# Optimization experiments

Measured on AMD Instinct MI355X. Metric: run time of the kernel, lower is better.

## Reference

```python
import jax, jax.numpy as jnp
import numpy as np
import math

NUM_GROUPS = 8
NUM_HEADS = 4
EPS = 1e-5


def group_norm(x, gamma, beta):
    B, C, H, W = x.shape
    g = x.reshape(B, NUM_GROUPS, C // NUM_GROUPS, H, W)
    mean = g.mean(axis=(2, 3, 4), keepdims=True)
    var = g.var(axis=(2, 3, 4), keepdims=True)
    g = (g - mean) * jax.lax.rsqrt(var + EPS)
    x = g.reshape(B, C, H, W)
    return x * gamma[None, :, None, None] + beta[None, :, None, None]


def setup_inputs() -> dict:
    key = jax.random.key(0)
    ks = jax.random.split(key, 4)
    B, C, H, W = 4, 256, 64, 64
    x = jax.random.normal(ks[0], (B, C, H, W), dtype=jnp.float32)
    gamma = jnp.ones((C,), dtype=jnp.float32)
    beta = jnp.zeros((C,), dtype=jnp.float32)
    w_qkv = jax.random.normal(ks[1], (3 * C, C), dtype=jnp.float32) / math.sqrt(C)
    b_qkv = jnp.zeros((3 * C,), dtype=jnp.float32)
    w_proj = jax.random.normal(ks[2], (C, C), dtype=jnp.float32) / math.sqrt(C)
    b_proj = jnp.zeros((C,), dtype=jnp.float32)
    return {"x": x, "gamma": gamma, "beta": beta, "w_qkv": w_qkv,
            "b_qkv": b_qkv, "w_proj": w_proj, "b_proj": b_proj}


def reference(x, gamma, beta, w_qkv, b_qkv, w_proj, b_proj):
    B, C, H, W = x.shape
    hd = C // NUM_HEADS  # head dim
    h = group_norm(x, gamma, beta)
    # 1x1 conv == per-pixel matmul: [B,3C,H,W]
    qkv = jnp.einsum('bchw,oc->bohw', h, w_qkv) + b_qkv[None, :, None, None]
    q, k, v = jnp.split(qkv, 3, axis=1)

    def shape(t):
        # [B,C,H,W] -> [B, heads, HW, hd]
        return t.reshape(B, NUM_HEADS, hd, H * W).transpose(0, 1, 3, 2)

    q, k, v = shape(q), shape(k), shape(v)
    attn = jnp.einsum('bhqd,bhkd->bhqk', q, k) * (1.0 / math.sqrt(hd))
    attn = jax.nn.softmax(attn, axis=-1)
    out = jnp.einsum('bhqk,bhkd->bhqd', attn, v)
    # [B, heads, HW, hd] -> [B, C, H, W]
    out = out.transpose(0, 1, 3, 2).reshape(B, C, H, W)
    out = jnp.einsum('bchw,oc->bohw', out, w_proj) + b_proj[None, :, None, None]
    return x + out
```

## Files before the change

### kernel.cpp

```cpp
#include <hip/hip_runtime.h>
#include <math.h>

#define NB 4
#define C_ 256
#define NG 8
#define CPG 32
#define HW 4096
#define NH 4
#define HD 64
#define EPS 1e-5f
#define QSCALE 0.1803368801111204f

typedef __attribute__((ext_vector_type(8))) short bf16x8_t;
typedef __attribute__((ext_vector_type(4))) float f32x4_t;
typedef const __attribute__((address_space(1))) void g_void;
typedef __attribute__((address_space(3))) void l_void;

__device__ __forceinline__ unsigned short f2bf(float f) {
    unsigned u = __float_as_uint(f);
    u += 0x7FFFu + ((u >> 16) & 1u);
    return (unsigned short)(u >> 16);
}

__device__ __forceinline__ unsigned cvtpk(float lo, float hi) {
    unsigned r;
    asm("v_cvt_pk_bf16_f32 %0, %1, %2" : "=v"(r) : "v"(lo), "v"(hi));
    return r;
}

__device__ __forceinline__ void plswap16(unsigned &a, unsigned &b) {
#if __has_builtin(__builtin_amdgcn_permlane16_swap)
    auto r = __builtin_amdgcn_permlane16_swap(a, b, false, false);
    a = r[0]; b = r[1];
#else
    unsigned as = (unsigned)__shfl_xor((int)a, 16);
    unsigned bs = (unsigned)__shfl_xor((int)b, 16);
    bool hi = (threadIdx.x & 16) != 0;
    unsigned na = hi ? bs : a;
    unsigned nb = hi ? b : as;
    a = na; b = nb;
#endif
}
__device__ __forceinline__ void plswap32(unsigned &a, unsigned &b) {
#if __has_builtin(__builtin_amdgcn_permlane32_swap)
    auto r = __builtin_amdgcn_permlane32_swap(a, b, false, false);
    a = r[0]; b = r[1];
#else
    unsigned as = (unsigned)__shfl_xor((int)a, 32);
    unsigned bs = (unsigned)__shfl_xor((int)b, 32);
    bool hi = (threadIdx.x & 32) != 0;
    unsigned na = hi ? bs : a;
    unsigned nb = hi ? b : as;
    a = na; b = nb;
#endif
}

__global__ __launch_bounds__(256) void gn_stats_wconv_k(const float* __restrict__ x,
                                                        float2* __restrict__ part,
                                                        const float* __restrict__ wq,
                                                        const float* __restrict__ wp,
                                                        unsigned short* __restrict__ wt,
                                                        unsigned short* __restrict__ wpt) {
    if (blockIdx.x >= 1024) {
        int i4 = (blockIdx.x - 1024) * 256 + threadIdx.x;
        const float* src;
        unsigned short* dst;
        int off;
        if (i4 < 49152) { src = wq; dst = wt; off = i4 * 4; }
        else            { src = wp; dst = wpt; off = (i4 - 49152) * 4; }
        float4 v = *(const float4*)(src + off);
        ushort4 o;
        o.x = f2bf(v.x); o.y = f2bf(v.y); o.z = f2bf(v.z); o.w = f2bf(v.w);
        *(ushort4*)(dst + off) = o;
        return;
    }
    int bg = blockIdx.x >> 5, ch = blockIdx.x & 31;
    const float4* base = (const float4*)(x + (size_t)bg * CPG * HW + ch * 4096);
    float s = 0.f, ss = 0.f;
    #pragma unroll
    for (int i = threadIdx.x; i < 1024; i += 256) {
        float4 v = base[i];
        s  += v.x + v.y + v.z + v.w;
        ss += v.x*v.x + v.y*v.y + v.z*v.z + v.w*v.w;
    }
    #pragma unroll
    for (int off = 32; off > 0; off >>= 1) {
        s  += __shfl_down(s, off);
        ss += __shfl_down(ss, off);
    }
    __shared__ float rs[4], rss[4];
    int wv = threadIdx.x >> 6;
    if ((threadIdx.x & 63) == 0) { rs[wv] = s; rss[wv] = ss; }
    __syncthreads();
    if (threadIdx.x == 0)
        part[blockIdx.x] = make_float2(rs[0]+rs[1]+rs[2]+rs[3], rss[0]+rss[1]+rss[2]+rss[3]);
}

__global__ __launch_bounds__(256) void gn_apply_t_k(const float* __restrict__ x,
                                                    const float* __restrict__ gamma,
                                                    const float* __restrict__ beta,
                                                    const float2* __restrict__ part,
                                                    unsigned short* __restrict__ ht) {
    __shared__ unsigned short T[64 * 66];
    __shared__ float sstat[4];
    int b = blockIdx.z, c0 = blockIdx.y * 64, p0 = blockIdx.x * 64;
    int t = threadIdx.x;
    if (t < 64) {
        int half = t >> 5;
        int g = b * NG + (c0 >> 5) + half;
        float2 v = part[g * 32 + (t & 31)];
        float s = v.x, ss = v.y;
        #pragma unroll
        for (int off = 16; off > 0; off >>= 1) {
            s  += __shfl_xor(s, off);
            ss += __shfl_xor(ss, off);
        }
        if ((t & 31) == 0) {
            const float inv = 1.f / (float)(CPG * HW);
            float mean = s * inv;
            float var  = ss * inv - mean * mean;
            sstat[half * 2]     = mean;
            sstat[half * 2 + 1] = rsqrtf(var + EPS);
        }
    }
    __syncthreads();
    int cr = t >> 4, pc = t & 15;
    #pragma unroll
    for (int cp = 0; cp < 4; cp++) {
        int c = c0 + cp * 16 + cr;
        int gl = (cp * 16 + cr) >> 5;
        float mean = sstat[gl * 2], rstd = sstat[gl * 2 + 1];
        float sc = gamma[c] * rstd;
        float sh = beta[c] - mean * sc;
        float4 v = *(const float4*)(x + ((size_t)(b * C_ + c)) * HW + p0 + pc * 4);
        int cc = cp * 16 + cr;
        T[(pc*4 + 0) * 66 + cc] = f2bf(v.x*sc + sh);
        T[(pc*4 + 1) * 66 + cc] = f2bf(v.y*sc + sh);
        T[(pc*4 + 2) * 66 + cc] = f2bf(v.z*sc + sh);
        T[(pc*4 + 3) * 66 + cc] = f2bf(v.w*sc + sh);
    }
    __syncthreads();
    int p = t >> 2, cq = t & 3;
    const unsigned* rp = (const unsigned*)(T + p * 66 + cq * 16);
    unsigned short* dst = ht + ((size_t)b * HW + p0 + p) * 256 + c0 + cq * 16;
    *(uint4*)dst       = make_uint4(rp[0], rp[1], rp[2], rp[3]);
    *(uint4*)(dst + 8) = make_uint4(rp[4], rp[5], rp[6], rp[7]);
}

__global__ __launch_bounds__(256) void gemm_qkv_mfma_k(const unsigned short* __restrict__ wt,
                                                       const unsigned short* __restrict__ ht,
                                                       const float* __restrict__ bias,
                                                       unsigned short* __restrict__ qt,
                                                       unsigned short* __restrict__ kt,
                                                       unsigned short* __restrict__ vv) {
    __shared__ unsigned short T[64 * 72];
    int b = blockIdx.z, my = blockIdx.y, px = blockIdx.x;
    int t = threadIdx.x, wave = t >> 6, lane = t & 63, quad = lane >> 4, l16 = lane & 15;
    int mw = wave & 1, pw = wave >> 1;
    const unsigned short* Ab = wt + (size_t)(my * 64 + mw * 32) * 256;
    const unsigned short* Bb = ht + ((size_t)b * HW + px * 64 + pw * 32) * 256;
    f32x4_t acc[2][2];
    const f32x4_t zz = {0.f, 0.f, 0.f, 0.f};
    acc[0][0] = zz; acc[0][1] = zz; acc[1][0] = zz; acc[1][1] = zz;
    #pragma unroll
    for (int kc = 0; kc < 8; kc++) {
        bf16x8_t af[2], bfr[2];
        #pragma unroll
        for (int mi = 0; mi < 2; mi++)
            af[mi] = *(const bf16x8_t*)(Ab + (mi*16 + l16) * 256 + kc*32 + quad*8);
        #pragma unroll
        for (int pi = 0; pi < 2; pi++)
            bfr[pi] = *(const bf16x8_t*)(Bb + (size_t)(pi*16 + l16) * 256 + kc*32 + quad*8);
        #pragma unroll
        for (int mi = 0; mi < 2; mi++)
            #pragma unroll
            for (int pi = 0; pi < 2; pi++)
                acc[mi][pi] = __builtin_amdgcn_mfma_f32_16x16x32_bf16(af[mi], bfr[pi], acc[mi][pi], 0, 0, 0);
    }
    int sec = my >> 2, hh = my & 3;
    if (sec < 2) {
        float scl = (sec == 0) ? QSCALE : 1.f;
        unsigned short* dst = ((sec == 0) ? qt : kt) + (size_t)(b * NH + hh) * HW * 64;
        #pragma unroll
        for (int mi = 0; mi < 2; mi++) {
            int d0 = mw*32 + mi*16 + quad*4;
            #pragma unroll
            for (int pi = 0; pi < 2; pi++) {
                int p = px*64 + pw*32 + pi*16 + l16;
                unsigned lo = cvtpk((acc[mi][pi][0] + bias[my*64 + d0 + 0]) * scl,
                                    (acc[mi][pi][1] + bias[my*64 + d0 + 1]) * scl);
                unsigned hi = cvtpk((acc[mi][pi][2] + bias[my*64 + d0 + 2]) * scl,
                                    (acc[mi][pi][3] + bias[my*64 + d0 + 3]) * scl);
                *(uint2*)(dst + (size_t)p * 64 + d0) = make_uint2(lo, hi);
            }
        }
    } else {
        unsigned short* dstv = vv + (size_t)(b * NH + hh) * 64 * HW;
        #pragma unroll
        for (int mi = 0; mi < 2; mi++)
            #pragma unroll
            for (int pi = 0; pi < 2; pi++) {
                int p = pw*32 + pi*16 + l16;
                #pragma unroll
                for (int r = 0; r < 4; r++) {
                    int d = mw*32 + mi*16 + quad*4 + r;
                    T[d * 72 + p] = f2bf(acc[mi][pi][r] + bias[my*64 + d]);
                }
            }
        __syncthreads();
        int dr = t >> 2, c4 = (t & 3) * 16;
        const unsigned* rp = (const unsigned*)(T + dr * 72 + c4);
        unsigned short* dd = dstv + (size_t)dr * HW + px * 64 + c4;
        *(uint4*)dd       = make_uint4(rp[0], rp[1], rp[2], rp[3]);
        *(uint4*)(dd + 8) = make_uint4(rp[4], rp[5], rp[6], rp[7]);
    }
}

__global__ __launch_bounds__(256) void gemm_proj_mfma_k(const unsigned short* __restrict__ wpt,
                                                        const unsigned short* __restrict__ ao,
                                                        const float* __restrict__ bias,
                                                        const float* __restrict__ x,
                                                        float* __restrict__ out) {
    int b = blockIdx.z, my = blockIdx.y, px = blockIdx.x;
    int t = threadIdx.x, wave = t >> 6, lane = t & 63, quad = lane >> 4, l16 = lane & 15;
    int mw = wave & 1, pw = wave >> 1;
    const unsigned short* Ab = wpt + (size_t)(my * 64 + mw * 32) * 256;
    const unsigned short* Bb = ao + ((size_t)b * HW + px * 64 + pw * 32) * 256;
    f32x4_t acc[2][2];
    const f32x4_t zz = {0.f, 0.f, 0.f, 0.f};
    acc[0][0] = zz; acc[0][1] = zz; acc[1][0] = zz; acc[1][1] = zz;
    #pragma unroll
    for (int kc = 0; kc < 8; kc++) {
        bf16x8_t af[2], bfr[2];
        #pragma unroll
        for (int mi = 0; mi < 2; mi++)
            af[mi] = *(const bf16x8_t*)(Ab + (mi*16 + l16) * 256 + kc*32 + quad*8);
        #pragma unroll
        for (int pi = 0; pi < 2; pi++)
            bfr[pi] = *(const bf16x8_t*)(Bb + (size_t)(pi*16 + l16) * 256 + kc*32 + quad*8);
        #pragma unroll
        for (int mi = 0; mi < 2; mi++)
            #pragma unroll
            for (int pi = 0; pi < 2; pi++)
                acc[mi][pi] = __builtin_amdgcn_mfma_f32_16x16x32_bf16(af[mi], bfr[pi], acc[mi][pi], 0, 0, 0);
    }
    #pragma unroll
    for (int mi = 0; mi < 2; mi++)
        #pragma unroll
        for (int pi = 0; pi < 2; pi++) {
            int p = px*64 + pw*32 + pi*16 + l16;
            #pragma unroll
            for (int r = 0; r < 4; r++) {
                int m = my*64 + mw*32 + mi*16 + quad*4 + r;
                size_t off = (size_t)(b * C_ + m) * HW + p;
                out[off] = acc[mi][pi][r] + bias[m] + x[off];
            }
        }
}

__global__ __launch_bounds__(512) __attribute__((amdgpu_waves_per_eu(2, 8)))
void attn_k(const unsigned short* __restrict__ qt,
            const unsigned short* __restrict__ kt,
            const unsigned short* __restrict__ vv,
            unsigned short* __restrict__ ao) {
    __shared__ __align__(16) unsigned short smem[24576];
    int t = threadIdx.x;
    int wave = t >> 6, lane = t & 63, quad = lane >> 4, l16 = lane & 15;
    int iw = wave & 3, jw = wave >> 2;
    int L = blockIdx.x;
    int W = (L & 7) * 64 + (L >> 3);
    int i0 = (W & 31) * 128;
    int hh = (W >> 5) & 3;
    int b  = W >> 7;
    const unsigned short* qb = qt + (size_t)(b * NH + hh) * HW * 64;
    const char* kbp = (const char*)(kt + (size_t)(b * NH + hh) * HW * 64);
    const char* vbp = (const char*)(vv + (size_t)(b * NH + hh) * 64 * HW);

    bf16x8_t qf[2][2];
    #pragma unroll
    for (int mi = 0; mi < 2; mi++)
        #pragma unroll
        for (int kc = 0; kc < 2; kc++)
            qf[mi][kc] = *(const bf16x8_t*)(qb + (size_t)(i0 + iw * 32 + mi * 16 + l16) * 64 + kc * 32 + quad * 8);

    f32x4_t oacc[4][2], osum[2];
    const f32x4_t zz = {0.f, 0.f, 0.f, 0.f};
    #pragma unroll
    for (int dt = 0; dt < 4; dt++) { oacc[dt][0] = zz; oacc[dt][1] = zz; }
    osum[0] = zz; osum[1] = zz;

    bf16x8_t ones;
    #pragma unroll
    for (int e = 0; e < 8; e++) ones[e] = (short)0x3F80;

    bool isK = (jw == 0);
    int soff[2], lbase[2];
    #pragma unroll
    for (int n = 0; n < 2; n++) {
        int s = (iw * 2 + n) * 64 + lane;
        int row = s >> 3;
        int c = (s & 7) ^ (row & 7);
        soff[n] = isK ? (row * 128 + c * 16) : (row * (HW * 2) + c * 16);
        lbase[n] = (isK ? 0 : 12288) + (iw * 2 + n) * 512;
    }
    const char* gsrc0 = isK ? kbp : vbp;
    int tstride = isK ? 8192 : 128;

    auto STAGE = [&](int tile, int buf) {
        const char* g = gsrc0 + (size_t)tile * tstride;
        #pragma unroll
        for (int n = 0; n < 2; n++)
            __builtin_amdgcn_global_load_lds((g_void*)(g + soff[n]),
                                             (l_void*)(smem + buf * 4096 + lbase[n]), 16, 0, 0);
    };

    STAGE(0, 0);
    STAGE(1, 1);

    int cur = 0;
    for (int jt = 0; jt < 64; jt++) {
        if (jt < 63) asm volatile("s_waitcnt vmcnt(2)" ::: "memory");
        else         asm volatile("s_waitcnt vmcnt(0)" ::: "memory");
        asm volatile("s_barrier" ::: "memory");
        if (jt + 2 < 64) {
            int nb = cur + 2; if (nb >= 3) nb -= 3;
            STAGE(jt + 2, nb);
        }
        const unsigned short* Kc = smem + cur * 4096;
        const unsigned short* Vc = smem + 12288 + cur * 4096;

        f32x4_t sacc[2][2];
        sacc[0][0] = zz; sacc[0][1] = zz; sacc[1][0] = zz; sacc[1][1] = zz;
        __builtin_amdgcn_s_setprio(1);
        #pragma unroll
        for (int nj = 0; nj < 2; nj++) {
            int j = jw * 32 + nj * 16 + l16;
            int rb = j * 8;
            bf16x8_t kf0 = *(const bf16x8_t*)&Kc[(rb + ((quad    ) ^ (j & 7))) * 8];
            bf16x8_t kf1 = *(const bf16x8_t*)&Kc[(rb + ((4 + quad) ^ (j & 7))) * 8];
            #pragma unroll
            for (int mi = 0; mi < 2; mi++) {
                sacc[mi][nj] = __builtin_amdgcn_mfma_f32_16x16x32_bf16(kf0, qf[mi][0], sacc[mi][nj], 0, 0, 0);
                sacc[mi][nj] = __builtin_amdgcn_mfma_f32_16x16x32_bf16(kf1, qf[mi][1], sacc[mi][nj], 0, 0, 0);
            }
        }
        __builtin_amdgcn_s_setprio(0);

        bf16x8_t pf[2];
        #pragma unroll
        for (int mi = 0; mi < 2; mi++) {
            #pragma unroll
            for (int nj = 0; nj < 2; nj++)
                #pragma unroll
                for (int r = 0; r < 4; r++)
                    sacc[mi][nj][r] = __builtin_amdgcn_exp2f(sacc[mi][nj][r]);

            unsigned lo0 = cvtpk(sacc[mi][0][0], sacc[mi][0][1]);
            unsigned hi0 = cvtpk(sacc[mi][0][2], sacc[mi][0][3]);
            unsigned lo1 = cvtpk(sacc[mi][1][0], sacc[mi][1][1]);
            unsigned hi1 = cvtpk(sacc[mi][1][2], sacc[mi][1][3]);
            plswap32(lo0, lo1); plswap16(lo0, lo1);
            plswap32(hi0, hi1); plswap16(hi0, hi1);
            union { unsigned u[4]; bf16x8_t v8; } pu;
            pu.u[0] = lo0; pu.u[1] = hi0; pu.u[2] = lo1; pu.u[3] = hi1;
            pf[mi] = pu.v8;
        }

        __builtin_amdgcn_s_setprio(1);
        #pragma unroll
        for (int dt = 0; dt < 4; dt++) {
            int d = dt * 16 + l16;
            bf16x8_t vf = *(const bf16x8_t*)&Vc[(d * 8 + ((jw * 4 + quad) ^ (d & 7))) * 8];
            oacc[dt][0] = __builtin_amdgcn_mfma_f32_16x16x32_bf16(vf, pf[0], oacc[dt][0], 0, 0, 0);
            oacc[dt][1] = __builtin_amdgcn_mfma_f32_16x16x32_bf16(vf, pf[1], oacc[dt][1], 0, 0, 0);
        }
        osum[0] = __builtin_amdgcn_mfma_f32_16x16x32_bf16(ones, pf[0], osum[0], 0, 0, 0);
        osum[1] = __builtin_amdgcn_mfma_f32_16x16x32_bf16(ones, pf[1], osum[1], 0, 0, 0);
        __builtin_amdgcn_s_setprio(0);

        cur = (cur + 1 == 3) ? 0 : cur + 1;
    }

    __syncthreads();
    float* Obuf = (float*)smem;
    if (jw == 1) {
        #pragma unroll
        for (int mi = 0; mi < 2; mi++) {
            int R = iw * 32 + mi * 16 + l16;
            #pragma unroll
            for (int dt = 0; dt < 4; dt++)
                *(f32x4_t*)&Obuf[R * 68 + dt * 16 + quad * 4] = oacc[dt][mi];
            if (quad == 0)
                Obuf[R * 68 + 64] = osum[mi][0];
        }
    }
    __syncthreads();
    if (jw == 0) {
        #pragma unroll
        for (int mi = 0; mi < 2; mi++) {
            int R = iw * 32 + mi * 16 + l16;
            float l  = osum[mi][0] + Obuf[R * 68 + 64];
            float c0 = 1.f / l;
            unsigned short* dst = ao + ((size_t)b * HW + i0 + R) * 256 + hh * 64 + quad * 4;
            #pragma unroll
            for (int dt = 0; dt < 4; dt++) {
                f32x4_t o1 = *(const f32x4_t*)&Obuf[R * 68 + dt * 16 + quad * 4];
                unsigned w0 = cvtpk((oacc[dt][mi][0] + o1[0]) * c0,
                                    (oacc[dt][mi][1] + o1[1]) * c0);
                unsigned w1 = cvtpk((oacc[dt][mi][2] + o1[2]) * c0,
                                    (oacc[dt][mi][3] + o1[3]) * c0);
                *(uint2*)(dst + dt * 16) = make_uint2(w0, w1);
            }
        }
    }
}

extern "C" void kernel_launch(void* const* d_in, const int* in_sizes, int n_in,
                              void* d_out, int out_size, void* d_ws, size_t ws_size,
                              hipStream_t stream) {
    const float* x      = (const float*)d_in[0];
    const float* gamma  = (const float*)d_in[1];
    const float* beta   = (const float*)d_in[2];
    const float* w_qkv  = (const float*)d_in[3];
    const float* b_qkv  = (const float*)d_in[4];
    const float* w_proj = (const float*)d_in[5];
    const float* b_proj = (const float*)d_in[6];
    float* out = (float*)d_out;

    float* stats = (float*)d_ws;
    float2* part = (float2*)(stats + 256);
    unsigned short* ht  = (unsigned short*)(stats + 256 + 2048);
    unsigned short* qt  = ht + (size_t)4194304;
    unsigned short* kt  = qt + (size_t)4194304;
    unsigned short* vv  = kt + (size_t)4194304;
    unsigned short* ao  = vv + (size_t)4194304;
    unsigned short* wt  = ao + (size_t)4194304;
    unsigned short* wpt = wt + 196608;

    gn_stats_wconv_k<<<1280, 256, 0, stream>>>(x, part, w_qkv, w_proj, wt, wpt);
    gn_apply_t_k<<<dim3(64, 4, NB), 256, 0, stream>>>(x, gamma, beta, part, ht);
    gemm_qkv_mfma_k<<<dim3(64, 12, NB), 256, 0, stream>>>(wt, ht, b_qkv, qt, kt, vv);
    attn_k<<<512, 512, 0, stream>>>(qt, kt, vv, ao);
    gemm_proj_mfma_k<<<dim3(64, 4, NB), 256, 0, stream>>>(wpt, ao, b_proj, x, out);
}
```

Baseline: 221.3 us.

## Retile QKV GEMM to 128x128 with LDS triple-buffered async loads

```diff
diff --git a/kernel.cpp b/kernel.cpp
--- a/kernel.cpp
+++ b/kernel.cpp
@@ -153,66 +153,116 @@
                                                        unsigned short* __restrict__ qt,
                                                        unsigned short* __restrict__ kt,
                                                        unsigned short* __restrict__ vv) {
-    __shared__ unsigned short T[64 * 72];
-    int b = blockIdx.z, my = blockIdx.y, px = blockIdx.x;
+    __shared__ __align__(16) unsigned short smem[24576];
     int t = threadIdx.x, wave = t >> 6, lane = t & 63, quad = lane >> 4, l16 = lane & 15;
-    int mw = wave & 1, pw = wave >> 1;
-    const unsigned short* Ab = wt + (size_t)(my * 64 + mw * 32) * 256;
-    const unsigned short* Bb = ht + ((size_t)b * HW + px * 64 + pw * 32) * 256;
-    f32x4_t acc[2][2];
+    int mq = wave & 1, pq = wave >> 1;
+    int L = blockIdx.x;
+    int W = (L & 7) * 96 + (L >> 3);
+    int b = W / 192;
+    int rem = W - b * 192;
+    int px = rem / 6;
+    int my = rem - px * 6;
+    const char* Ag = (const char*)(wt + (size_t)(my * 128) * 256);
+    const char* Bg = (const char*)(ht + ((size_t)b * HW + px * 128) * 256);
+
+    int soff[2], lbs[2];
+    #pragma unroll
+    for (int n = 0; n < 2; n++) {
+        int s = n * 256 + t;
+        int row = s >> 2, c = (s & 3) ^ (row & 3);
+        soff[n] = row * 512 + c * 16;
+        lbs[n]  = s * 8;
+    }
+
+    auto STAGE = [&](int kc, int buf) {
+        const char* a  = Ag + kc * 64;
+        const char* bb = Bg + kc * 64;
+        #pragma unroll
+        for (int n = 0; n < 2; n++) {
+            __builtin_amdgcn_global_load_lds((g_void*)(a  + soff[n]), (l_void*)(smem + buf * 8192 + lbs[n]), 16, 0, 0);
+            __builtin_amdgcn_global_load_lds((g_void*)(bb + soff[n]), (l_void*)(smem + buf * 8192 + 4096 + lbs[n]), 16, 0, 0);
+        }
+    };
+
+    f32x4_t acc[4][4];
     const f32x4_t zz = {0.f, 0.f, 0.f, 0.f};
-    acc[0][0] = zz; acc[0][1] = zz; acc[1][0] = zz; acc[1][1] = zz;
-    #pragma unroll
+    #pragma unroll
+    for (int i = 0; i < 4; i++)
+        #pragma unroll
+        for (int j = 0; j < 4; j++) acc[i][j] = zz;
+
+    STAGE(0, 0);
+    STAGE(1, 1);
+    int cur = 0;
     for (int kc = 0; kc < 8; kc++) {
-        bf16x8_t af[2], bfr[2];
-        #pragma unroll
-        for (int mi = 0; mi < 2; mi++)
-            af[mi] = *(const bf16x8_t*)(Ab + (mi*16 + l16) * 256 + kc*32 + quad*8);
-        #pragma unroll
-        for (int pi = 0; pi < 2; pi++)
-            bfr[pi] = *(const bf16x8_t*)(Bb + (size_t)(pi*16 + l16) * 256 + kc*32 + quad*8);
-        #pragma unroll
-        for (int mi = 0; mi < 2; mi++)
-            #pragma unroll
-            for (int pi = 0; pi < 2; pi++)
+        if (kc < 7) asm volatile("s_waitcnt vmcnt(4)" ::: "memory");
+        else        asm volatile("s_waitcnt vmcnt(0)" ::: "memory");
+        asm volatile("s_barrier" ::: "memory");
+        if (kc + 2 < 8) { int nb = cur + 2; if (nb >= 3) nb -= 3; STAGE(kc + 2, nb); }
+        const unsigned short* Ac = smem + cur * 8192;
+        const unsigned short* Bc = smem + cur * 8192 + 4096;
+        bf16x8_t af[4], bfr[4];
+        #pragma unroll
+        for (int mi = 0; mi < 4; mi++) {
+            int R = mq * 64 + mi * 16 + l16;
+            af[mi] = *(const bf16x8_t*)&Ac[(R * 4 + (quad ^ (R & 3))) * 8];
+        }
+        #pragma unroll
+        for (int pi = 0; pi < 4; pi++) {
+            int P = pq * 64 + pi * 16 + l16;
+            bfr[pi] = *(const bf16x8_t*)&Bc[(P * 4 + (quad ^ (P & 3))) * 8];
+        }
+        __builtin_amdgcn_s_setprio(1);
+        #pragma unroll
+        for (int mi = 0; mi < 4; mi++)
+            #pragma unroll
+            for (int pi = 0; pi < 4; pi++)
                 acc[mi][pi] = __builtin_amdgcn_mfma_f32_16x16x32_bf16(af[mi], bfr[pi], acc[mi][pi], 0, 0, 0);
-    }
-    int sec = my >> 2, hh = my & 3;
+        __builtin_amdgcn_s_setprio(0);
+        cur = (cur + 1 == 3) ? 0 : cur + 1;
+    }
+
+    int sec = my >> 1;
+    int hh = ((my & 1) << 1) | mq;
     if (sec < 2) {
         float scl = (sec == 0) ? QSCALE : 1.f;
         unsigned short* dst = ((sec == 0) ? qt : kt) + (size_t)(b * NH + hh) * HW * 64;
         #pragma unroll
-        for (int mi = 0; mi < 2; mi++) {
-            int d0 = mw*32 + mi*16 + quad*4;
-            #pragma unroll
-            for (int pi = 0; pi < 2; pi++) {
-                int p = px*64 + pw*32 + pi*16 + l16;
-                unsigned lo = cvtpk((acc[mi][pi][0] + bias[my*64 + d0 + 0]) * scl,
-                                    (acc[mi][pi][1] + bias[my*64 + d0 + 1]) * scl);
-                unsigned hi = cvtpk((acc[mi][pi][2] + bias[my*64 + d0 + 2]) * scl,
-                                    (acc[mi][pi][3] + bias[my*64 + d0 + 3]) * scl);
+        for (int mi = 0; mi < 4; mi++) {
+            int d0 = mi * 16 + quad * 4;
+            int mg = my * 128 + mq * 64 + d0;
+            #pragma unroll
+            for (int pi = 0; pi < 4; pi++) {
+                int p = px * 128 + pq * 64 + pi * 16 + l16;
+                unsigned lo = cvtpk((acc[mi][pi][0] + bias[mg + 0]) * scl,
+                                    (acc[mi][pi][1] + bias[mg + 1]) * scl);
+                unsigned hi = cvtpk((acc[mi][pi][2] + bias[mg + 2]) * scl,
+                                    (acc[mi][pi][3] + bias[mg + 3]) * scl);
                 *(uint2*)(dst + (size_t)p * 64 + d0) = make_uint2(lo, hi);
             }
         }
     } else {
-        unsigned short* dstv = vv + (size_t)(b * NH + hh) * 64 * HW;
-        #pragma unroll
-        for (int mi = 0; mi < 2; mi++)
-            #pragma unroll
-            for (int pi = 0; pi < 2; pi++) {
-                int p = pw*32 + pi*16 + l16;
+        __syncthreads();
+        unsigned short* T = smem;
+        #pragma unroll
+        for (int mi = 0; mi < 4; mi++) {
+            int dT = mq * 64 + mi * 16 + quad * 4;
+            int mg = my * 128 + dT;
+            #pragma unroll
+            for (int pi = 0; pi < 4; pi++) {
+                int pl = pq * 64 + pi * 16 + l16;
                 #pragma unroll
-                for (int r = 0; r < 4; r++) {
-                    int d = mw*32 + mi*16 + quad*4 + r;
-                    T[d * 72 + p] = f2bf(acc[mi][pi][r] + bias[my*64 + d]);
-                }
+                for (int r = 0; r < 4; r++)
+                    T[(dT + r) * 130 + pl] = f2bf(acc[mi][pi][r] + bias[mg + r]);
             }
+        }
         __syncthreads();
-        int dr = t >> 2, c4 = (t & 3) * 16;
-        const unsigned* rp = (const unsigned*)(T + dr * 72 + c4);
-        unsigned short* dd = dstv + (size_t)dr * HW + px * 64 + c4;
-        *(uint4*)dd       = make_uint4(rp[0], rp[1], rp[2], rp[3]);
-        *(uint4*)(dd + 8) = make_uint4(rp[4], rp[5], rp[6], rp[7]);
+        int dT = t >> 1, half = t & 1;
+        const unsigned* rp = (const unsigned*)(T + dT * 130 + half * 64);
+        unsigned short* dd = vv + ((size_t)(b * 256 + (my & 1) * 128 + dT)) * HW + px * 128 + half * 64;
+        #pragma unroll
+        for (int q8 = 0; q8 < 8; q8++)
+            *(uint4*)(dd + q8 * 8) = make_uint4(rp[q8*4+0], rp[q8*4+1], rp[q8*4+2], rp[q8*4+3]);
     }
 }
 
@@ -439,7 +489,7 @@
 
     gn_stats_wconv_k<<<1280, 256, 0, stream>>>(x, part, w_qkv, w_proj, wt, wpt);
     gn_apply_t_k<<<dim3(64, 4, NB), 256, 0, stream>>>(x, gamma, beta, part, ht);
-    gemm_qkv_mfma_k<<<dim3(64, 12, NB), 256, 0, stream>>>(wt, ht, b_qkv, qt, kt, vv);
+    gemm_qkv_mfma_k<<<768, 256, 0, stream>>>(wt, ht, b_qkv, qt, kt, vv);
     attn_k<<<512, 512, 0, stream>>>(qt, kt, vv, ao);
     gemm_proj_mfma_k<<<dim3(64, 4, NB), 256, 0, stream>>>(wpt, ao, b_proj, x, out);
 }
```

Result: faster. 190.5 us (-13.9%).
